# Optimization experiments

Hardware: AMD Instinct MI355X
Metric: run time of the kernel (lower is better)

## Reference

```python
import jax, jax.numpy as jnp
import numpy as np

D_IN = 1024
D_OUT = 1024
SEQ = 4096


def setup_inputs() -> dict:
    key = jax.random.key(0)
    kx, kq, kk, kv = jax.random.split(key, 4)
    s = 1.0 / np.sqrt(D_IN)
    return {
        "x": jax.random.normal(kx, (SEQ, D_IN), dtype=jnp.float32),
        # torch Linear weights: shape [d_out, d_in], y = x @ W.T
        "Wq": jax.random.uniform(kq, (D_OUT, D_IN), jnp.float32, -s, s),
        "Wk": jax.random.uniform(kk, (D_OUT, D_IN), jnp.float32, -s, s),
        "Wv": jax.random.uniform(kv, (D_OUT, D_IN), jnp.float32, -s, s),
    }


def reference(x, Wq, Wk, Wv):
    # QKV projections (no bias)
    q = x @ Wq.T  # [N, d_out]
    k = x @ Wk.T
    v = x @ Wv.T
    scale = 1.0 / jnp.sqrt(jnp.asarray(k.shape[-1], x.dtype))
    att = jax.nn.softmax((q @ k.T) * scale, axis=-1)  # [N, N]
    return att @ v  # [N, d_out]
```

## Files before the change

kernel.cpp:

```cpp
#include <hip/hip_runtime.h>
#include <hip/hip_bf16.h>
#include <math.h>

typedef __attribute__((ext_vector_type(8))) short short8;
typedef __attribute__((ext_vector_type(4))) float floatx4;

static __device__ __forceinline__ unsigned short f2bf(float f) {
    union { float f; unsigned int u; } a; a.f = f;
    unsigned int u = a.u;
    return (unsigned short)((u + 0x7FFFu + ((u >> 16) & 1u)) >> 16);
}
static __device__ __forceinline__ float bf2f(unsigned short h) {
    union { unsigned int u; float f; } a; a.u = ((unsigned int)h) << 16;
    return a.f;
}

static __device__ __forceinline__ void cvt8(const float* __restrict__ src,
                                            unsigned short* __restrict__ dst, int i) {
    float4 v0 = *(const float4*)(src + i);
    float4 v1 = *(const float4*)(src + i + 4);
    ushort4 o0, o1;
    o0.x = f2bf(v0.x); o0.y = f2bf(v0.y); o0.z = f2bf(v0.z); o0.w = f2bf(v0.w);
    o1.x = f2bf(v1.x); o1.y = f2bf(v1.y); o1.z = f2bf(v1.z); o1.w = f2bf(v1.w);
    *(ushort4*)(dst + i) = o0;
    *(ushort4*)(dst + i + 4) = o1;
}

struct CV { const float* x; unsigned short* xb;
            const float* W[3]; unsigned short* Wb[3]; float* l; };
__global__ __launch_bounds__(256)
void cvt_all(CV a) {
    int b = blockIdx.x, t = threadIdx.x;
    if (b < 2048) {
        cvt8(a.x, a.xb, (b * 256 + t) * 8);
    } else if (b < 3584) {
        int z  = (b - 2048) >> 9;
        int bb = (b - 2048) & 511;
        cvt8(a.W[z], a.Wb[z], (bb * 256 + t) * 8);
    } else {
        float4 zz = {0.f, 0.f, 0.f, 0.f};
        #pragma unroll
        for (int c = 0; c < 4; c++)
            *(float4*)(a.l + t * 16 + c * 4) = zz;
    }
}

#define DSR(dst, base, OFF)                                                    \
    asm volatile("ds_read_b128 %0, %1 offset:%2"                               \
                 : "=v"(dst) : "v"(base), "n"(OFF))
#define LGKM(N) asm volatile("s_waitcnt lgkmcnt(" #N ")" ::: "memory")
#define SBAR()  asm volatile("s_barrier" ::: "memory")

typedef __attribute__((address_space(3))) char* lds3p;

__device__ __forceinline__ void gemm256_core(
    const unsigned short* __restrict__ A, const unsigned short* __restrict__ B,
    int lda, int k_begin, int bm, int bn,
    unsigned short* lds, floatx4 (&acc)[8][4])
{
    const int t    = threadIdx.x;
    const int wave = t >> 6;
    const int lane = t & 63;
    const int wrow = wave >> 2;
    const int wcol = wave & 3;
    const int lm   = lane & 15;
    const int ce8  = (((lane >> 4) ^ ((lm >> 1) & 3)) << 3);

    const int srow = t >> 2;
    const int gsh  = (((t & 3) ^ ((srow >> 1) & 3)) << 3);
    const unsigned short* srcA = A + (size_t)(bm + srow) * lda + k_begin + gsh;
    const unsigned short* srcB = B + (size_t)(bn + srow) * lda + k_begin + gsh;
    const size_t rstep = (size_t)128 * lda;
    char* ldsc = (char*)lds;
    const int w1k = wave << 10;

    lds3p lp3 = (lds3p)lds;
    lds3p va = lp3 + (((wrow << 7) + lm) * 64 + (ce8 << 1));
    lds3p vb = lp3 + (65536 + ((wcol << 6) + lm) * 64 + (ce8 << 1));

#define STAGE(kind, kh, tau) do {                                              \
        int taue_ = (tau) >= 16 ? (tau) - 2 : (tau);   \
        int ko_ = (taue_ << 6) + ((kh) << 5);                                  \
        unsigned lo_ = ((kind) << 16) + (((tau) & 1) << 15) + ((kh) << 14) + w1k; \
        const unsigned short* s_ = ((kind) ? srcB : srcA) + ko_;               \
        __builtin_amdgcn_global_load_lds(                                      \
            (const __attribute__((address_space(1))) void*)s_,                 \
            (__attribute__((address_space(3))) void*)(ldsc + lo_), 16, 0, 0);  \
        __builtin_amdgcn_global_load_lds(                                      \
            (const __attribute__((address_space(1))) void*)(s_ + rstep),       \
            (__attribute__((address_space(3))) void*)(ldsc + lo_ + 8192), 16, 0, 0); \
    } while (0)

#define MFMA4(R, AV)                                                           \
    do {                                                                       \
        acc[R][0] = __builtin_amdgcn_mfma_f32_16x16x32_bf16(AV, b4[0], acc[R][0], 0, 0, 0); \
        acc[R][1] = __builtin_amdgcn_mfma_f32_16x16x32_bf16(AV, b4[1], acc[R][1], 0, 0, 0); \
        acc[R][2] = __builtin_amdgcn_mfma_f32_16x16x32_bf16(AV, b4[2], acc[R][2], 0, 0, 0); \
        acc[R][3] = __builtin_amdgcn_mfma_f32_16x16x32_bf16(AV, b4[3], acc[R][3], 0, 0, 0); \
    } while (0)

    STAGE(1, 0, 0); STAGE(0, 0, 0); STAGE(1, 1, 0); STAGE(0, 1, 0);
    STAGE(1, 0, 1); STAGE(0, 0, 1); STAGE(1, 1, 1);
    asm volatile("s_waitcnt vmcnt(6)" ::: "memory");
    SBAR();

    short8 na[4], b4[4];
    for (int t2 = 0; t2 < 16; t2 += 2) {
        #pragma unroll
        for (int s = 0; s < 8; s++) {
            const int hi = s >> 2;
            const int s4 = s & 3;
            const int ks = s4 >> 1, ih = s4 & 1;
            const int tc = t2 + hi;
            constexpr int DB = 32768, KH = 16384, FR = 1024;
            const int PB = hi * DB + ks * KH;
            if (s4 == 0 || s4 == 2) {
                DSR(b4[0], vb, PB + 0 * FR);
                DSR(b4[1], vb, PB + 1 * FR);
                DSR(b4[2], vb, PB + 2 * FR);
                DSR(b4[3], vb, PB + 3 * FR);
            }
            DSR(na[0], va, PB + (ih * 4 + 0) * FR);
            DSR(na[1], va, PB + (ih * 4 + 1) * FR);
            DSR(na[2], va, PB + (ih * 4 + 2) * FR);
            DSR(na[3], va, PB + (ih * 4 + 3) * FR);
            if      (s4 == 0) STAGE(0, 1, tc + 1);
            else if (s4 == 1) STAGE(1, 0, tc + 2);
            else if (s4 == 2) STAGE(0, 0, tc + 2);
            else              STAGE(1, 1, tc + 2);
            __builtin_amdgcn_s_setprio(1);
            LGKM(3); __builtin_amdgcn_sched_barrier(0);
            MFMA4(ih * 4 + 0, na[0]);
            LGKM(2); __builtin_amdgcn_sched_barrier(0);
            MFMA4(ih * 4 + 1, na[1]);
            LGKM(1); __builtin_amdgcn_sched_barrier(0);
            MFMA4(ih * 4 + 2, na[2]);
            LGKM(0); __builtin_amdgcn_sched_barrier(0);
            MFMA4(ih * 4 + 3, na[3]);
            __builtin_amdgcn_s_setprio(0);
            if (s4 == 3) asm volatile("s_waitcnt vmcnt(6)" ::: "memory");
            SBAR();
        }
    }
#undef STAGE
#undef MFMA4
}

__device__ __forceinline__ void tile_store256(unsigned short* sm,
                                              floatx4 (&acc)[8][4], float scale, int trans,
                                              unsigned short* __restrict__ C, int ldc,
                                              int rbase, int cbase)
{
    const int t = threadIdx.x, wave = t >> 6, lane = t & 63;
    const int wrow = wave >> 2, wcol = wave & 3;
    const int lm = lane & 15, rq = ((lane >> 4) << 2);
    #pragma unroll
    for (int h = 0; h < 2; h++) {
        __syncthreads();
        if (!trans) {
            if (wrow == h) {
                #pragma unroll
                for (int i = 0; i < 8; i++)
                    #pragma unroll
                    for (int j = 0; j < 4; j++)
                        #pragma unroll
                        for (int r = 0; r < 4; r++)
                            sm[(i * 16 + rq + r) * 264 + wcol * 64 + j * 16 + lm] =
                                f2bf(acc[i][j][r] * scale);
            }
        } else {
            if ((wcol >> 1) == h) {
                #pragma unroll
                for (int i = 0; i < 8; i++)
                    #pragma unroll
                    for (int j = 0; j < 4; j++) {
                        ushort4 v;
                        v.x = f2bf(acc[i][j][0] * scale);
                        v.y = f2bf(acc[i][j][1] * scale);
                        v.z = f2bf(acc[i][j][2] * scale);
                        v.w = f2bf(acc[i][j][3] * scale);
                        *(ushort4*)&sm[((wcol & 1) * 64 + j * 16 + lm) * 264 +
                                       wrow * 128 + i * 16 + rq] = v;
                    }
            }
        }
        __syncthreads();
        #pragma unroll
        for (int p = 0; p < 4; p++) {
            int row = p * 32 + (t >> 4);
            int c0  = (t & 15) * 8;
            *(short8*)&C[(size_t)(rbase + h * 128 + row) * ldc + cbase + c0] =
                *(const short8*)&sm[row * 264 + c0];
            *(short8*)&C[(size_t)(rbase + h * 128 + row) * ldc + cbase + c0 + 128] =
                *(const short8*)&sm[row * 264 + c0 + 128];
        }
    }
}

struct P3 { const unsigned short* W[3]; unsigned short* O[3]; };
__global__ __launch_bounds__(512, 2)
void proj3(const unsigned short* __restrict__ xb, P3 a) {
    __shared__ __align__(16) unsigned short lds[65536];
    const int lid = blockIdx.x;
    const int xcd = lid & 7, rem = lid >> 3;
    const int z   = rem >> 3;
    const int idx = xcd * 8 + (rem & 7);
    const int by = idx >> 2, bx = idx & 3;
    const int bm = by * 256, bn = bx * 256;

    floatx4 acc[8][4];
    #pragma unroll
    for (int i = 0; i < 8; i++)
        #pragma unroll
        for (int j = 0; j < 4; j++) { floatx4 zz = {0.f,0.f,0.f,0.f}; acc[i][j] = zz; }

    gemm256_core(xb, a.W[z], 1024, 0, bm, bn, lds, acc);

    const int trans = (z == 2);
    const float scale = (z == 0) ? 0.03125f : 1.0f;
    tile_store256(lds, acc, scale, trans, a.O[z],
                  trans ? 4096 : 1024, trans ? bn : bm, trans ? bm : bn);
}

__global__ __launch_bounds__(512, 2)
void gemm_ps(const unsigned short* __restrict__ q, const unsigned short* __restrict__ k,
             unsigned short* __restrict__ Pm, float* __restrict__ l) {
    __shared__ __align__(16) unsigned short lds[65536];
    const int lid = blockIdx.x;
    const int xcd = lid & 7, r32 = lid >> 3;
    const int by = ((xcd >> 1) << 2) + (r32 & 3);
    const int bx = ((xcd & 1) << 3) + (r32 >> 2);
    const int bm = by * 256, bn = bx * 256;

    floatx4 acc[8][4];
    #pragma unroll
    for (int i = 0; i < 8; i++)
        #pragma unroll
        for (int j = 0; j < 4; j++) { floatx4 zz = {0.f,0.f,0.f,0.f}; acc[i][j] = zz; }

    gemm256_core(q, k, 1024, 0, bm, bn, lds, acc);

    const int lane = threadIdx.x & 63, wave = threadIdx.x >> 6;
    const int wrow = wave >> 2;
    const int lm = lane & 15, rq = ((lane >> 4) << 2);
    #pragma unroll
    for (int i = 0; i < 8; i++) {
        #pragma unroll
        for (int r = 0; r < 4; r++) {
            float rs = 0.f;
            #pragma unroll
            for (int j = 0; j < 4; j++) {
                float e = __expf(acc[i][j][r]);
                acc[i][j][r] = e;
                rs += e;
            }
            rs += __shfl_xor(rs, 1);
            rs += __shfl_xor(rs, 2);
            rs += __shfl_xor(rs, 4);
            rs += __shfl_xor(rs, 8);
            if (lm == 0) atomicAdd(l + bm + wrow * 128 + i * 16 + rq + r, rs);
        }
    }
    tile_store256(lds, acc, 1.0f, 0, Pm, 4096, bm, bn);
}

__global__ __launch_bounds__(512, 2)
void gemm_osplit(const unsigned short* __restrict__ Pm, const unsigned short* __restrict__ vT,
                 unsigned short* __restrict__ Opart) {
    __shared__ __align__(16) unsigned short lds[65536];
    const int lid = blockIdx.x;
    const int xcd = lid & 7, r32 = lid >> 3;
    const int z   = r32 & 3;
    const int idx = (r32 >> 2) * 8 + xcd;
    const int by = idx >> 2, bx = idx & 3;

    floatx4 acc[8][4];
    #pragma unroll
    for (int i = 0; i < 8; i++)
        #pragma unroll
        for (int j = 0; j < 4; j++) { floatx4 zz = {0.f,0.f,0.f,0.f}; acc[i][j] = zz; }

    gemm256_core(Pm, vT, 4096, z * 1024, by * 256, bx * 256, lds, acc);

    tile_store256(lds, acc, 1.0f, 0, Opart + (size_t)z * (4096 * 1024), 1024,
                  by * 256, bx * 256);
}

__global__ __launch_bounds__(256)
void reduce_scale(const unsigned short* __restrict__ Op, const float* __restrict__ l,
                  float* __restrict__ out) {
    int i = (blockIdx.x * 256 + threadIdx.x) * 4;
    ushort4 a = *(const ushort4*)(Op + i);
    ushort4 b = *(const ushort4*)(Op + 4194304 + i);
    ushort4 c = *(const ushort4*)(Op + 8388608 + i);
    ushort4 d = *(const ushort4*)(Op + 12582912 + i);
    float inv = 1.0f / l[i >> 10];
    float4 o;
    o.x = (bf2f(a.x) + bf2f(b.x) + bf2f(c.x) + bf2f(d.x)) * inv;
    o.y = (bf2f(a.y) + bf2f(b.y) + bf2f(c.y) + bf2f(d.y)) * inv;
    o.z = (bf2f(a.z) + bf2f(b.z) + bf2f(c.z) + bf2f(d.z)) * inv;
    o.w = (bf2f(a.w) + bf2f(b.w) + bf2f(c.w) + bf2f(d.w)) * inv;
    *(float4*)(out + i) = o;
}

extern "C" void kernel_launch(void* const* d_in, const int* in_sizes, int n_in,
                              void* d_out, int out_size, void* d_ws, size_t ws_size,
                              hipStream_t stream) {
    const float* x  = (const float*)d_in[0];
    const float* Wq = (const float*)d_in[1];
    const float* Wk = (const float*)d_in[2];
    const float* Wv = (const float*)d_in[3];
    float* out = (float*)d_out;

    char* ws = (char*)d_ws;
    const size_t MB = 1u << 20;
    unsigned short* vTb = (unsigned short*)(ws);
    unsigned short* xb  = (unsigned short*)(ws + 8 * MB);
    unsigned short* Wqb = (unsigned short*)(ws + 16 * MB);
    unsigned short* Wkb = (unsigned short*)(ws + 18 * MB);
    unsigned short* Wvb = (unsigned short*)(ws + 20 * MB);
    unsigned short* qb  = (unsigned short*)(ws + 22 * MB);
    unsigned short* kb  = (unsigned short*)(ws + 30 * MB);
    unsigned short* P   = (unsigned short*)(ws + 40 * MB);
    float*          l   = (float*)(ws + 72 * MB);
    unsigned short* Opart = (unsigned short*)(ws + 8 * MB);

    dim3 b256(256), b512(512);
    CV cv = {x, xb, {Wq, Wk, Wv}, {Wqb, Wkb, Wvb}, l};
    cvt_all<<<dim3(3585), b256, 0, stream>>>(cv);

    P3 p3 = {{Wqb, Wkb, Wvb}, {qb, kb, vTb}};
    proj3<<<dim3(192), b512, 0, stream>>>(xb, p3);

    gemm_ps<<<dim3(256), b512, 0, stream>>>(qb, kb, P, l);

    gemm_osplit<<<dim3(256), b512, 0, stream>>>(P, vTb, Opart);

    reduce_scale<<<dim3(4096), b256, 0, stream>>>(Opart, l, out);
}
```

Before: 195.9 us.

## Fuse projection, score, PV and reduce kernels into one persistent kernel with grid barriers

Replaces four separate launches (proj3, gemm_ps, gemm_osplit, reduce_scale) with one 256-block persistent kernel that runs the stages back to back, separated by a software grid barrier built from atomic counters. The goal is to remove the launch gaps and tail drain between the stages. The barrier counters are zeroed in the conversion kernel. The approach relies on all 256 blocks being resident at once (two blocks per CU), otherwise it deadlocks. Spin-waiting at the barrier also adds its own synchronisation cost.

```diff
diff --git a/kernel.cpp b/kernel.cpp
--- a/kernel.cpp
+++ b/kernel.cpp
@@ -42,7 +42,30 @@
         #pragma unroll
         for (int c = 0; c < 4; c++)
             *(float4*)(a.l + t * 16 + c * 4) = zz;
-    }
+        if (t == 0) {
+            ((unsigned*)(a.l + 4096))[0] = 0;
+            ((unsigned*)(a.l + 4096))[1] = 0;
+        }
+    }
+}
+
+__device__ __forceinline__ void grid_barrier(unsigned* cnt, unsigned* gen,
+                                             unsigned nblk) {
+    __threadfence();
+    __syncthreads();
+    if (threadIdx.x == 0) {
+        unsigned g = atomicAdd(gen, 0u);
+        if (atomicAdd(cnt, 1u) == nblk - 1u) {
+            atomicExch(cnt, 0u);
+            __threadfence();
+            atomicAdd(gen, 1u);
+        } else {
+            while (atomicAdd(gen, 0u) == g)
+                __builtin_amdgcn_s_sleep(2);
+        }
+    }
+    __syncthreads();
+    __threadfence();
 }
 
 #define DSR(dst, base, OFF)                                                    \
@@ -110,10 +133,10 @@
         for (int s = 0; s < 8; s++) {
             const int hi = s >> 2;
             const int s4 = s & 3;
-            const int ks = s4 >> 1, ih = s4 & 1;
+            const int ih = s4 & 1;
             const int tc = t2 + hi;
             constexpr int DB = 32768, KH = 16384, FR = 1024;
-            const int PB = hi * DB + ks * KH;
+            const int PB = hi * DB + (s4 >> 1) * KH;
             if (s4 == 0 || s4 == 2) {
                 DSR(b4[0], vb, PB + 0 * FR);
                 DSR(b4[1], vb, PB + 1 * FR);
@@ -142,6 +165,7 @@
             SBAR();
         }
     }
+    LGKM(0);
 #undef STAGE
 #undef MFMA4
 }
@@ -197,110 +221,120 @@
     }
 }
 
-struct P3 { const unsigned short* W[3]; unsigned short* O[3]; };
+struct MegaA {
+    const unsigned short* xb;
+    const unsigned short* W[3];
+    unsigned short* O[3];
+    unsigned short* Pm;
+    float* l;
+    unsigned short* Opart;
+    float* out;
+    unsigned* cnt;
+    unsigned* gen;
+};
 __global__ __launch_bounds__(512, 2)
-void proj3(const unsigned short* __restrict__ xb, P3 a) {
+void mega(MegaA a) {
     __shared__ __align__(16) unsigned short lds[65536];
     const int lid = blockIdx.x;
-    const int xcd = lid & 7, rem = lid >> 3;
-    const int z   = rem >> 3;
-    const int idx = xcd * 8 + (rem & 7);
-    const int by = idx >> 2, bx = idx & 3;
-    const int bm = by * 256, bn = bx * 256;
-
-    floatx4 acc[8][4];
-    #pragma unroll
-    for (int i = 0; i < 8; i++)
-        #pragma unroll
-        for (int j = 0; j < 4; j++) { floatx4 zz = {0.f,0.f,0.f,0.f}; acc[i][j] = zz; }
-
-    gemm256_core(xb, a.W[z], 1024, 0, bm, bn, lds, acc);
-
-    const int trans = (z == 2);
-    const float scale = (z == 0) ? 0.03125f : 1.0f;
-    tile_store256(lds, acc, scale, trans, a.O[z],
-                  trans ? 4096 : 1024, trans ? bn : bm, trans ? bm : bn);
-}
-
-__global__ __launch_bounds__(512, 2)
-void gemm_ps(const unsigned short* __restrict__ q, const unsigned short* __restrict__ k,
-             unsigned short* __restrict__ Pm, float* __restrict__ l) {
-    __shared__ __align__(16) unsigned short lds[65536];
-    const int lid = blockIdx.x;
-    const int xcd = lid & 7, r32 = lid >> 3;
-    const int by = ((xcd >> 1) << 2) + (r32 & 3);
-    const int bx = ((xcd & 1) << 3) + (r32 >> 2);
-    const int bm = by * 256, bn = bx * 256;
-
-    floatx4 acc[8][4];
-    #pragma unroll
-    for (int i = 0; i < 8; i++)
-        #pragma unroll
-        for (int j = 0; j < 4; j++) { floatx4 zz = {0.f,0.f,0.f,0.f}; acc[i][j] = zz; }
-
-    gemm256_core(q, k, 1024, 0, bm, bn, lds, acc);
-
-    const int lane = threadIdx.x & 63, wave = threadIdx.x >> 6;
-    const int wrow = wave >> 2;
-    const int lm = lane & 15, rq = ((lane >> 4) << 2);
-    #pragma unroll
-    for (int i = 0; i < 8; i++) {
-        #pragma unroll
-        for (int r = 0; r < 4; r++) {
-            float rs = 0.f;
+
+    if (lid < 192) {
+        const int xcd = lid & 7, rem = lid >> 3;
+        const int z   = rem >> 3;
+        const int idx = xcd * 8 + (rem & 7);
+        const int by = idx >> 2, bx = idx & 3;
+        const int bm = by * 256, bn = bx * 256;
+
+        floatx4 acc[8][4];
+        #pragma unroll
+        for (int i = 0; i < 8; i++)
             #pragma unroll
-            for (int j = 0; j < 4; j++) {
-                float e = __expf(acc[i][j][r]);
-                acc[i][j][r] = e;
-                rs += e;
+            for (int j = 0; j < 4; j++) { floatx4 zz = {0.f,0.f,0.f,0.f}; acc[i][j] = zz; }
+
+        gemm256_core(a.xb, a.W[z], 1024, 0, bm, bn, lds, acc);
+
+        const int trans = (z == 2);
+        const float scale = (z == 0) ? 0.03125f : 1.0f;
+        tile_store256(lds, acc, scale, trans, a.O[z],
+                      trans ? 4096 : 1024, trans ? bn : bm, trans ? bm : bn);
+    }
+    grid_barrier(a.cnt, a.gen, 256);
+
+    {
+        const int xcd = lid & 7, r32 = lid >> 3;
+        const int by = ((xcd >> 1) << 2) + (r32 & 3);
+        const int bx = ((xcd & 1) << 3) + (r32 >> 2);
+        const int bm = by * 256, bn = bx * 256;
+
+        floatx4 acc[8][4];
+        #pragma unroll
+        for (int i = 0; i < 8; i++)
+            #pragma unroll
+            for (int j = 0; j < 4; j++) { floatx4 zz = {0.f,0.f,0.f,0.f}; acc[i][j] = zz; }
+
+        gemm256_core(a.O[0], a.O[1], 1024, 0, bm, bn, lds, acc);
+
+        const int lane = threadIdx.x & 63, wave = threadIdx.x >> 6;
+        const int wrow = wave >> 2;
+        const int lm = lane & 15, rq = ((lane >> 4) << 2);
+        #pragma unroll
+        for (int i = 0; i < 8; i++) {
+            #pragma unroll
+            for (int r = 0; r < 4; r++) {
+                float rs = 0.f;
+                #pragma unroll
+                for (int j = 0; j < 4; j++) {
+                    float e = __expf(acc[i][j][r]);
+                    acc[i][j][r] = e;
+                    rs += e;
+                }
+                rs += __shfl_xor(rs, 1);
+                rs += __shfl_xor(rs, 2);
+                rs += __shfl_xor(rs, 4);
+                rs += __shfl_xor(rs, 8);
+                if (lm == 0) atomicAdd(a.l + bm + wrow * 128 + i * 16 + rq + r, rs);
             }
-            rs += __shfl_xor(rs, 1);
-            rs += __shfl_xor(rs, 2);
-            rs += __shfl_xor(rs, 4);
-            rs += __shfl_xor(rs, 8);
-            if (lm == 0) atomicAdd(l + bm + wrow * 128 + i * 16 + rq + r, rs);
-        }
-    }
-    tile_store256(lds, acc, 1.0f, 0, Pm, 4096, bm, bn);
-}
-
-__global__ __launch_bounds__(512, 2)
-void gemm_osplit(const unsigned short* __restrict__ Pm, const unsigned short* __restrict__ vT,
-                 unsigned short* __restrict__ Opart) {
-    __shared__ __align__(16) unsigned short lds[65536];
-    const int lid = blockIdx.x;
-    const int xcd = lid & 7, r32 = lid >> 3;
-    const int z   = r32 & 3;
-    const int idx = (r32 >> 2) * 8 + xcd;
-    const int by = idx >> 2, bx = idx & 3;
-
-    floatx4 acc[8][4];
-    #pragma unroll
-    for (int i = 0; i < 8; i++)
-        #pragma unroll
-        for (int j = 0; j < 4; j++) { floatx4 zz = {0.f,0.f,0.f,0.f}; acc[i][j] = zz; }
-
-    gemm256_core(Pm, vT, 4096, z * 1024, by * 256, bx * 256, lds, acc);
-
-    tile_store256(lds, acc, 1.0f, 0, Opart + (size_t)z * (4096 * 1024), 1024,
-                  by * 256, bx * 256);
-}
-
-__global__ __launch_bounds__(256)
-void reduce_scale(const unsigned short* __restrict__ Op, const float* __restrict__ l,
-                  float* __restrict__ out) {
-    int i = (blockIdx.x * 256 + threadIdx.x) * 4;
-    ushort4 a = *(const ushort4*)(Op + i);
-    ushort4 b = *(const ushort4*)(Op + 4194304 + i);
-    ushort4 c = *(const ushort4*)(Op + 8388608 + i);
-    ushort4 d = *(const ushort4*)(Op + 12582912 + i);
-    float inv = 1.0f / l[i >> 10];
-    float4 o;
-    o.x = (bf2f(a.x) + bf2f(b.x) + bf2f(c.x) + bf2f(d.x)) * inv;
-    o.y = (bf2f(a.y) + bf2f(b.y) + bf2f(c.y) + bf2f(d.y)) * inv;
-    o.z = (bf2f(a.z) + bf2f(b.z) + bf2f(c.z) + bf2f(d.z)) * inv;
-    o.w = (bf2f(a.w) + bf2f(b.w) + bf2f(c.w) + bf2f(d.w)) * inv;
-    *(float4*)(out + i) = o;
+        }
+        tile_store256(lds, acc, 1.0f, 0, a.Pm, 4096, bm, bn);
+    }
+    grid_barrier(a.cnt, a.gen, 256);
+
+    {
+        const int xcd = lid & 7, r32 = lid >> 3;
+        const int z   = r32 & 3;
+        const int idx = (r32 >> 2) * 8 + xcd;
+        const int by = idx >> 2, bx = idx & 3;
+
+        floatx4 acc[8][4];
+        #pragma unroll
+        for (int i = 0; i < 8; i++)
+            #pragma unroll
+            for (int j = 0; j < 4; j++) { floatx4 zz = {0.f,0.f,0.f,0.f}; acc[i][j] = zz; }
+
+        gemm256_core(a.Pm, a.O[2], 4096, z * 1024, by * 256, bx * 256, lds, acc);
+
+        tile_store256(lds, acc, 1.0f, 0, a.Opart + (size_t)z * (4096 * 1024), 1024,
+                      by * 256, bx * 256);
+    }
+    grid_barrier(a.cnt, a.gen, 256);
+
+    {
+        const int t = threadIdx.x;
+        #pragma unroll
+        for (int c = 0; c < 8; c++) {
+            int i = (c * 131072 + lid * 512 + t) * 4;
+            ushort4 p0 = *(const ushort4*)(a.Opart + i);
+            ushort4 p1 = *(const ushort4*)(a.Opart + 4194304 + i);
+            ushort4 p2 = *(const ushort4*)(a.Opart + 8388608 + i);
+            ushort4 p3 = *(const ushort4*)(a.Opart + 12582912 + i);
+            float inv = 1.0f / a.l[i >> 10];
+            float4 o;
+            o.x = (bf2f(p0.x) + bf2f(p1.x) + bf2f(p2.x) + bf2f(p3.x)) * inv;
+            o.y = (bf2f(p0.y) + bf2f(p1.y) + bf2f(p2.y) + bf2f(p3.y)) * inv;
+            o.z = (bf2f(p0.z) + bf2f(p1.z) + bf2f(p2.z) + bf2f(p3.z)) * inv;
+            o.w = (bf2f(p0.w) + bf2f(p1.w) + bf2f(p2.w) + bf2f(p3.w)) * inv;
+            *(float4*)(a.out + i) = o;
+        }
+    }
 }
 
 extern "C" void kernel_launch(void* const* d_in, const int* in_sizes, int n_in,
@@ -323,18 +357,19 @@
     unsigned short* kb  = (unsigned short*)(ws + 30 * MB);
     unsigned short* P   = (unsigned short*)(ws + 40 * MB);
     float*          l   = (float*)(ws + 72 * MB);
+    unsigned* cnt = (unsigned*)(ws + 72 * MB + 16384);
+    unsigned* gen = cnt + 1;
     unsigned short* Opart = (unsigned short*)(ws + 8 * MB);
 
     dim3 b256(256), b512(512);
     CV cv = {x, xb, {Wq, Wk, Wv}, {Wqb, Wkb, Wvb}, l};
     cvt_all<<<dim3(3585), b256, 0, stream>>>(cv);
 
-    P3 p3 = {{Wqb, Wkb, Wvb}, {qb, kb, vTb}};
-    proj3<<<dim3(192), b512, 0, stream>>>(xb, p3);
-
-    gemm_ps<<<dim3(256), b512, 0, stream>>>(qb, kb, P, l);
-
-    gemm_osplit<<<dim3(256), b512, 0, stream>>>(P, vTb, Opart);
-
-    reduce_scale<<<dim3(4096), b256, 0, stream>>>(Opart, l, out);
-}
+    MegaA ma;
+    ma.xb = xb;
+    ma.W[0] = Wqb; ma.W[1] = Wkb; ma.W[2] = Wvb;
+    ma.O[0] = qb;  ma.O[1] = kb;  ma.O[2] = vTb;
+    ma.Pm = P; ma.l = l; ma.Opart = Opart; ma.out = out;
+    ma.cnt = cnt; ma.gen = gen;
+    mega<<<dim3(256), b512, 0, stream>>>(ma);
+}
```

Result: slower. 486.2 us (+148.1%).
